# Kernel optimization log

Measured on AMD Instinct MI355X. Metric: run time of the kernel, lower is better.

## Reference

```python
import jax, jax.numpy as jnp
import numpy as np

B, S, D, H = 2, 2048, 2048, 16
HD = D // H  # 128


def setup_inputs() -> dict:
    key = jax.random.key(0)
    ks = jax.random.split(key, 6)
    sc = 0.02
    return {
        "x": jax.random.normal(ks[0], (B, S, D), jnp.float32),
        "attention_mask": jnp.ones((B, S), jnp.int32),
        "w_qkv": jax.random.normal(ks[1], (D, 3 * D), jnp.float32) * sc,
        "b_qkv": jnp.zeros((3 * D,), jnp.float32),
        "w_o": jax.random.normal(ks[2], (D, D), jnp.float32) * sc,
        "b_o": jnp.zeros((D,), jnp.float32),
        "ln1_w": jnp.ones((D,), jnp.float32),
        "w1": jax.random.normal(ks[3], (D, 8 * D), jnp.float32) * sc,
        "b1": jnp.zeros((8 * D,), jnp.float32),
        "w2": jax.random.normal(ks[4], (4 * D, D), jnp.float32) * sc,
        "b2": jnp.zeros((D,), jnp.float32),
        "ln2_w": jnp.ones((D,), jnp.float32),
    }


def rmsnorm(x, w, eps=1e-6):
    rms = jnp.sqrt(jnp.mean(x * x, axis=-1, keepdims=True) + eps)
    return w * (x / rms)


def rope_tables(seq_len, dim, base=10000.0):
    inv_freq = 1.0 / (base ** (jnp.arange(0, dim, 2, dtype=jnp.float32) / dim))
    t = jnp.arange(seq_len, dtype=jnp.float32)
    freqs = t[:, None] * inv_freq[None, :]          # [S, dim/2]
    emb = jnp.concatenate([freqs, freqs], axis=-1)  # [S, dim]
    return jnp.cos(emb), jnp.sin(emb)


def apply_rope(x, cos, sin):
    # Faithful to source: rotate pairs, then out = rot*cos + roll(rot,1)*sin
    xr = x.reshape(*x.shape[:-1], -1, 2)
    x1, x2 = xr[..., 0], xr[..., 1]
    rot = jnp.stack([-x2, x1], axis=-1).reshape(x.shape)
    return rot * cos + jnp.roll(rot, shift=1, axis=-1) * sin


def transformer_layer(x, attention_mask, w_qkv, b_qkv, w_o, b_o, ln1_w, w1, b1, w2, b2, ln2_w):
    residual = x
    qkv = x @ w_qkv + b_qkv                         # [B,S,3D]
    q, k, v = jnp.split(qkv, 3, axis=-1)
    split = lambda t: t.reshape(B, S, H, HD).transpose(0, 2, 1, 3)  # [B,H,S,HD]
    q, k, v = split(q), split(k), split(v)

    cos, sin = rope_tables(S, HD)                   # [S,HD], broadcasts over B,H
    q = apply_rope(q, cos, sin)
    k = apply_rope(k, cos, sin)

    scores = jnp.einsum("bhqd,bhkd->bhqk", q, k) / jnp.sqrt(jnp.float32(HD))
    mask = (attention_mask == 1)[:, None, None, :]  # [B,1,1,S]
    scores = jnp.where(mask, scores, -jnp.inf)
    attn = jax.nn.softmax(scores, axis=-1)
    out = jnp.einsum("bhqk,bhkd->bhqd", attn, v)
    out = out.transpose(0, 2, 1, 3).reshape(B, S, D)
    out = out @ w_o + b_o

    x = rmsnorm(out + residual, ln1_w)
    residual = x
    h = x @ w1 + b1                                 # [B,S,8D]
    h, gate = jnp.split(h, 2, axis=-1)
    h = h * jax.nn.gelu(gate, approximate=False)
    h = h @ w2 + b2
    return rmsnorm(h + residual, ln2_w)


def reference(x, attention_mask, w_qkv, b_qkv, w_o, b_o, ln1_w, w1, b1, w2, b2, ln2_w):
    return transformer_layer(x, attention_mask, w_qkv, b_qkv, w_o, b_o, ln1_w, w1, b1, w2, b2, ln2_w)
```

## Files before the change

### kernel.cpp

```cpp
#include <hip/hip_runtime.h>
#include <cstdint>

typedef unsigned short u16;
typedef __attribute__((ext_vector_type(8))) short short8;
typedef __attribute__((ext_vector_type(8))) unsigned short ushortx8;
typedef __attribute__((ext_vector_type(4))) float floatx4;

#define DEV __device__ __forceinline__

DEV u16 f2bf(float f) {
  union { float f; uint32_t u; } x; x.f = f;
  uint32_t r = x.u + 0x7fffu + ((x.u >> 16) & 1u);
  return (u16)(r >> 16);
}
DEV float bf2f(u16 h) {
  union { float f; uint32_t u; } x; x.u = ((uint32_t)h) << 16;
  return x.f;
}
DEV float fast_gelu(float g) {
  float u = 0.7978845608f * (g + 0.044715f * g * g * g);
  float e = __expf(-2.0f * fabsf(u));
  float th = (1.0f - e) / (1.0f + e);
  th = (u < 0.0f) ? -th : th;
  return 0.5f * g * (1.0f + th);
}
DEV void gload_lds16(const void* g, void* lds) {
  __builtin_amdgcn_global_load_lds(
      (const __attribute__((address_space(1))) char*)(uintptr_t)g,
      (__attribute__((address_space(3))) char*)(uintptr_t)lds, 16, 0, 0);
}


__global__ __launch_bounds__(256) void k_cvt_bf16(const float* __restrict__ in,
                                                  u16* __restrict__ out, int n) {
  int i = (blockIdx.x * 256 + threadIdx.x) * 4;
  if (i + 3 < n) {
    float4 v = *(const float4*)(in + i);
    ushort4 o;
    o.x = f2bf(v.x); o.y = f2bf(v.y); o.z = f2bf(v.z); o.w = f2bf(v.w);
    *(ushort4*)(out + i) = o;
  }
}

__global__ __launch_bounds__(256) void k_transpose_all(const float* __restrict__ Wq,
                                                       u16* __restrict__ WqT,
                                                       const float* __restrict__ Wo,
                                                       u16* __restrict__ WoT,
                                                       const float* __restrict__ W2,
                                                       u16* __restrict__ W2T) {
  __shared__ u16 t[32][33];
  int id = blockIdx.x;
  const float* W; u16* Wt; int R, C, tix;
  if (id < 12288)      { W = Wq; Wt = WqT; R = 2048; C = 6144; tix = id; }
  else if (id < 16384) { W = Wo; Wt = WoT; R = 2048; C = 2048; tix = id - 12288; }
  else                 { W = W2; Wt = W2T; R = 8192; C = 2048; tix = id - 16384; }
  int ntc = C >> 5;
  int c0 = (tix % ntc) * 32, r0 = (tix / ntc) * 32;
  int tx = threadIdx.x & 31, ty = threadIdx.x >> 5;
#pragma unroll
  for (int i = ty; i < 32; i += 8)
    t[i][tx] = f2bf(W[(size_t)(r0 + i) * C + c0 + tx]);
  __syncthreads();
#pragma unroll
  for (int i = ty; i < 32; i += 8)
    Wt[(size_t)(c0 + i) * R + r0 + tx] = t[tx][i];
}

__global__ __launch_bounds__(256) void k_transpose_w1p(const float* __restrict__ W,
                                                       u16* __restrict__ Wt) {
  __shared__ u16 t[32][33];
  int tx = threadIdx.x & 31, ty = threadIdx.x >> 5;
  int r0 = blockIdx.y * 32;
  int c0 = blockIdx.x * 32;
  int eta = c0 + tx;
  int Bq = eta >> 8, i = eta & 255, wn = (i >> 6) & 3, r = i & 63, n = r >> 4, tt = r & 15;
  int src = Bq * 128 + wn * 32 + (n & 1) * 16 + tt + ((n >= 2) ? 8192 : 0);
#pragma unroll
  for (int k = ty; k < 32; k += 8)
    t[k][tx] = f2bf(W[(size_t)(r0 + k) * 16384 + src]);
  __syncthreads();
#pragma unroll
  for (int i2 = ty; i2 < 32; i2 += 8)
    Wt[(size_t)(c0 + i2) * 2048 + r0 + tx] = t[tx][i2];
}

__global__ __launch_bounds__(256) void k_rope_tab(float* __restrict__ ct, float* __restrict__ st) {
  int i = blockIdx.x * 256 + threadIdx.x;
  int s = i >> 6, j = i & 63;
  float invf = 1.0f / powf(10000.0f, (float)j * (1.0f / 64.0f));
  float ang = (float)s * invf;
  ct[i] = cosf(ang);
  st[i] = sinf(ang);
}

__global__ __launch_bounds__(256) void k_rope_split(const u16* __restrict__ qkv,
                                                    const float* __restrict__ ct,
                                                    const float* __restrict__ st,
                                                    u16* __restrict__ qr, u16* __restrict__ kr) {
  int bs = blockIdx.x;
  int b = bs >> 11, s = bs & 2047;
  __shared__ float q[2048], k[2048];
  const u16* row = qkv + (size_t)bs * 6144;
  for (int i = threadIdx.x * 4; i < 2048; i += 1024) {
    ushort4 qa = *(const ushort4*)(row + i);
    ushort4 ka = *(const ushort4*)(row + 2048 + i);
    q[i] = bf2f(qa.x); q[i + 1] = bf2f(qa.y); q[i + 2] = bf2f(qa.z); q[i + 3] = bf2f(qa.w);
    k[i] = bf2f(ka.x); k[i + 1] = bf2f(ka.y); k[i + 2] = bf2f(ka.z); k[i + 3] = bf2f(ka.w);
  }
  __syncthreads();
  int i0 = threadIdx.x * 8;
  int h = i0 >> 7, d0 = i0 & 127;
  const float* qh = q + (h << 7);
  const float* kh = k + (h << 7);
  ushortx8 qo, ko;
#pragma unroll
  for (int e = 0; e < 8; ++e) {
    int d = d0 + e;
    int dm1 = (d + 127) & 127;
    float c = ct[(s << 6) + (d & 63)];
    float sn = st[(s << 6) + (d & 63)];
    float rq  = (d & 1)   ? qh[d - 1]   : -qh[d + 1];
    float rq1 = (dm1 & 1) ? qh[dm1 - 1] : -qh[dm1 + 1];
    float rk  = (d & 1)   ? kh[d - 1]   : -kh[d + 1];
    float rk1 = (dm1 & 1) ? kh[dm1 - 1] : -kh[dm1 + 1];
    qo[e] = f2bf(rq * c + rq1 * sn);
    ko[e] = f2bf(rk * c + rk1 * sn);
  }
  size_t obase = (((size_t)b * 16 + h) * 2048 + s) * 128 + d0;
  *(ushortx8*)(qr + obase) = qo;
  *(ushortx8*)(kr + obase) = ko;
}

__global__ __launch_bounds__(256) void k_v_transpose(const u16* __restrict__ qkv,
                                                     u16* __restrict__ vt) {
  __shared__ u16 t[32][33];
  int tx = threadIdx.x & 31, ty = threadIdx.x >> 5;
  int s0 = blockIdx.x * 32;
  int dm0 = (blockIdx.y & 63) * 32;
  int b = blockIdx.y >> 6;
#pragma unroll
  for (int i = ty; i < 32; i += 8)
    t[i][tx] = qkv[((size_t)(b * 2048) + s0 + i) * 6144 + 4096 + dm0 + tx];
  __syncthreads();
#pragma unroll
  for (int i = ty; i < 32; i += 8)
    vt[((size_t)b * 2048 + dm0 + i) * 2048 + s0 + tx] = t[tx][i];
}

template <int EPI>
__global__ __launch_bounds__(512, 2) void k_gemm256(const u16* __restrict__ A,
                                                    const u16* __restrict__ Bt,
                                                    void* __restrict__ C,
                                                    const float* __restrict__ bias,
                                                    int M, int N, int K, int nsplit) {
  __shared__ __align__(16) u16 lds[4][2][8192];
  const int tid = threadIdx.x;
  const int w = tid >> 6, lane = tid & 63;
  const int l15 = lane & 15, l4 = lane >> 4;
  const int wm = w >> 2, wn = w & 3;
  const int nbn = N >> 8;
  const int nbm = M >> 8;

  int bm, bn, split = 0;
  if (nsplit == 1 && nbm == 16 && (nbn & 7) == 0) {
    const int xcd = blockIdx.x & 7, l = blockIdx.x >> 3;
    const int xr = xcd >> 1, xc = xcd & 1;
    const int stn = l >> 4, lbm = (l >> 2) & 3, lbn = l & 3;
    bm = xr * 4 + lbm;
    bn = xc * (nbn >> 1) + stn * 4 + lbn;
  } else {
    const int nwg = gridDim.x;
    const int q = nwg >> 3, r8 = nwg & 7;
    const int xcd = blockIdx.x & 7, loc = blockIdx.x >> 3;
    const int swz = (xcd < r8 ? xcd * (q + 1) : r8 * (q + 1) + (xcd - r8) * q) + loc;
    const int ntiles = nwg / nsplit;
    split = swz / ntiles;
    const int tix = swz % ntiles;
    bm = tix / nbn; bn = tix % nbn;
  }
  const int klen = K / nsplit;
  const int kofs = split * klen;

  const size_t abase = (size_t)bm * 256 * K + kofs;
  const size_t bbase = (size_t)bn * 256 * K + kofs;
  const int nt = klen >> 5;

  const int sr = tid >> 2;
  const int sc = (tid & 3) ^ ((sr >> 1) & 3);
  auto stage = [&](int kt, int li, int op) {
    const u16* src = op ? (Bt + bbase) : (A + abase);
    gload_lds16(src + (size_t)(li * 128 + sr) * K + kt * 32 + sc * 8,
                (void*)&lds[kt & 3][op][(li * 512 + w * 64) * 8]);
  };

  const int fro = l15 * 32 + (l4 ^ ((l15 >> 1) & 3)) * 8;

  floatx4 acc[8][4];
  floatx4 zero = {0.f, 0.f, 0.f, 0.f};
#pragma unroll
  for (int m = 0; m < 8; ++m)
#pragma unroll
    for (int n = 0; n < 4; ++n) acc[m][n] = zero;

  for (int kt = 0; kt < 3; ++kt)
    if (kt < nt) {
      stage(kt, 0, 0); stage(kt, 0, 1);
      stage(kt, 1, 0); stage(kt, 1, 1);
    }

  for (int t = 0; t < nt; ++t) {
    const int buf = t & 3;
    if (t < nt - 2)       asm volatile("s_waitcnt vmcnt(8)" ::: "memory");
    else if (t == nt - 2) asm volatile("s_waitcnt vmcnt(4)" ::: "memory");
    else                  asm volatile("s_waitcnt vmcnt(0)" ::: "memory");
    __builtin_amdgcn_sched_barrier(0);
    __builtin_amdgcn_s_barrier();
    const u16* Ab = &lds[buf][0][wm * 4096 + fro];
    const u16* Bb = &lds[buf][1][wn * 2048 + fro];
    short8 av[4], bv[4];
#pragma unroll
    for (int n = 0; n < 4; ++n) bv[n] = *(const short8*)(Bb + n * 512);
#pragma unroll
    for (int i = 0; i < 4; ++i) av[i] = *(const short8*)(Ab + i * 512);
    if (t + 3 < nt) { stage(t + 3, 0, 0); stage(t + 3, 0, 1); }
    asm volatile("s_waitcnt lgkmcnt(0)" ::: "memory");
    __builtin_amdgcn_sched_barrier(0);
    __builtin_amdgcn_s_setprio(1);
#pragma unroll
    for (int i = 0; i < 4; ++i)
#pragma unroll
      for (int n = 0; n < 4; ++n)
        acc[i][n] = __builtin_amdgcn_mfma_f32_16x16x32_bf16(av[i], bv[n], acc[i][n], 0, 0, 0);
    __builtin_amdgcn_s_setprio(0);
    __builtin_amdgcn_s_barrier();
#pragma unroll
    for (int i = 0; i < 4; ++i) av[i] = *(const short8*)(Ab + (4 + i) * 512);
    if (t + 3 < nt) { stage(t + 3, 1, 0); stage(t + 3, 1, 1); }
    asm volatile("s_waitcnt lgkmcnt(0)" ::: "memory");
    __builtin_amdgcn_sched_barrier(0);
    __builtin_amdgcn_s_setprio(1);
#pragma unroll
    for (int i = 0; i < 4; ++i)
#pragma unroll
      for (int n = 0; n < 4; ++n)
        acc[4 + i][n] = __builtin_amdgcn_mfma_f32_16x16x32_bf16(av[i], bv[n], acc[4 + i][n], 0, 0, 0);
    __builtin_amdgcn_s_setprio(0);
  }

  const int row0 = bm * 256 + wm * 128, col0 = bn * 256 + wn * 64;
  if (EPI == 2) {
    float* P = (float*)C + (size_t)split * M * N;
#pragma unroll
    for (int n = 0; n < 4; ++n) {
      int col = col0 + n * 16 + l15;
#pragma unroll
      for (int m = 0; m < 8; ++m)
#pragma unroll
        for (int j = 0; j < 4; ++j) {
          int row = row0 + m * 16 + l4 * 4 + j;
          P[(size_t)row * N + col] = acc[m][n][j];
        }
    }
  } else if (EPI == 3) {
    __syncthreads();
    u16* ep = ((u16*)lds) + w * 4096;
    const int colA = bn * 128 + wn * 32;
#pragma unroll
    for (int n = 0; n < 2; ++n) {
      float ba = bias[colA + n * 16 + l15];
      float bg = bias[8192 + colA + n * 16 + l15];
#pragma unroll
      for (int m = 0; m < 8; ++m)
#pragma unroll
        for (int j = 0; j < 4; ++j) {
          float a = acc[m][n][j] + ba;
          float g = acc[m][n + 2][j] + bg;
          ep[(m * 16 + l4 * 4 + j) * 32 + n * 16 + l15] = f2bf(a * fast_gelu(g));
        }
    }
    const int rr = lane >> 2, cg = lane & 3;
    u16* Cg = (u16*)C;
    const int Nact = N >> 1;
#pragma unroll
    for (int pass = 0; pass < 8; ++pass) {
      short8 v = *(const short8*)&ep[(pass * 16 + rr) * 32 + cg * 8];
      size_t grow = row0 + pass * 16 + rr;
      *(short8*)&Cg[grow * Nact + colA + cg * 8] = v;
    }
  } else {
    __syncthreads();
    u16* ep = ((u16*)lds) + w * 8192;
#pragma unroll
    for (int n = 0; n < 4; ++n) {
      float bb = bias[col0 + n * 16 + l15];
#pragma unroll
      for (int m = 0; m < 8; ++m)
#pragma unroll
        for (int j = 0; j < 4; ++j)
          ep[(m * 16 + l4 * 4 + j) * 64 + n * 16 + l15] = f2bf(acc[m][n][j] + bb);
    }
    const int rr = lane >> 3, cg = lane & 7;
    u16* Cg = (u16*)C;
#pragma unroll
    for (int pass = 0; pass < 16; ++pass) {
      short8 v = *(const short8*)&ep[(pass * 8 + rr) * 64 + cg * 8];
      size_t grow = row0 + pass * 8 + rr;
      *(short8*)&Cg[grow * N + col0 + cg * 8] = v;
    }
  }
}

__global__ __launch_bounds__(512, 4) void k_attn(const u16* __restrict__ Qr,
                                                 const u16* __restrict__ Kr,
                                                 const u16* __restrict__ Vt,
                                                 const int* __restrict__ mask,
                                                 u16* __restrict__ O) {
  constexpr int S = 2048, HD = 128, H = 16;
  __shared__ __align__(16) u16 Ksh[64 * 128];
  __shared__ __align__(16) u16 Vsh[128 * 64];
  __shared__ __align__(16) u16 Psh[8][16 * 72];
  __shared__ float Msh[2048];

  const int bid = blockIdx.x;
  const int xcd = bid & 7, local = bid >> 3;
  const int bh = xcd * 4 + (local >> 4);
  const int qt = local & 15;
  const int b = bh >> 4, h = bh & 15;
  const int tid = threadIdx.x, wave = tid >> 6, lane = tid & 63;
  const int l15 = lane & 15, l4 = lane >> 4;
  const size_t bhs = (size_t)(b * H + h);
  const u16* Qb = Qr + bhs * S * HD;
  const u16* Kb = Kr + bhs * S * HD;
  const u16* Vb = Vt + bhs * HD * S;

  for (int i = tid; i < 2048; i += 512)
    Msh[i] = (mask[b * S + i] == 1) ? 0.0f : -1e30f;

  const int qrow = qt * 128 + wave * 16 + l15;
  short8 qf[4];
#pragma unroll
  for (int kk = 0; kk < 4; ++kk)
    qf[kk] = *(const short8*)&Qb[(size_t)qrow * HD + kk * 32 + l4 * 8];

  float m_run[4], l_run[4];
  floatx4 o_acc[8];
  floatx4 zero = {0.f, 0.f, 0.f, 0.f};
#pragma unroll
  for (int j = 0; j < 4; ++j) { m_run[j] = -1e30f; l_run[j] = 0.f; }
#pragma unroll
  for (int n = 0; n < 8; ++n) o_acc[n] = zero;

  for (int ktile = 0; ktile < S / 64; ++ktile) {
    __syncthreads();
#pragma unroll
    for (int it = 0; it < 2; ++it) {
      int gi = it * 512 + tid;
      {
        int row = gi >> 4, g = gi & 15;
        int gs = (g & 8) | ((g ^ row) & 7);
        gload_lds16(Kb + (size_t)(ktile * 64 + row) * HD + gs * 8,
                    (char*)&Ksh[it * 4096 + wave * 512]);
      }
      {
        int row = gi >> 3, g = gi & 7;
        int gs = (g ^ row) & 7;
        gload_lds16(Vb + (size_t)row * S + ktile * 64 + gs * 8,
                    (char*)&Vsh[it * 4096 + wave * 512]);
      }
    }
    __syncthreads();

    floatx4 s_acc[4];
#pragma unroll
    for (int nf = 0; nf < 4; ++nf) s_acc[nf] = zero;
    __builtin_amdgcn_s_setprio(1);
#pragma unroll
    for (int kk = 0; kk < 4; ++kk) {
#pragma unroll
      for (int nf = 0; nf < 4; ++nf) {
        int key = nf * 16 + l15;
        int G = kk * 4 + l4;
        int lg = (G & 8) | ((G ^ key) & 7);
        short8 kv = *(const short8*)&Ksh[key * 128 + lg * 8];
        s_acc[nf] = __builtin_amdgcn_mfma_f32_16x16x32_bf16(qf[kk], kv, s_acc[nf], 0, 0, 0);
      }
    }
    __builtin_amdgcn_s_setprio(0);

    const float scale = 0.08838834764831845f;
    float p[4][4];
#pragma unroll
    for (int nf = 0; nf < 4; ++nf) {
      float ma = Msh[ktile * 64 + nf * 16 + l15];
#pragma unroll
      for (int j = 0; j < 4; ++j) p[nf][j] = s_acc[nf][j] * scale + ma;
    }
#pragma unroll
    for (int j = 0; j < 4; ++j) {
      float mx = fmaxf(fmaxf(p[0][j], p[1][j]), fmaxf(p[2][j], p[3][j]));
      mx = fmaxf(mx, __shfl_xor(mx, 1));
      mx = fmaxf(mx, __shfl_xor(mx, 2));
      mx = fmaxf(mx, __shfl_xor(mx, 4));
      mx = fmaxf(mx, __shfl_xor(mx, 8));
      float mnew = fmaxf(m_run[j], mx);
      float corr = __expf(m_run[j] - mnew);
      float ps = 0.f;
#pragma unroll
      for (int nf = 0; nf < 4; ++nf) {
        p[nf][j] = __expf(p[nf][j] - mnew);
        ps += p[nf][j];
      }
      l_run[j] = l_run[j] * corr + ps;
      m_run[j] = mnew;
#pragma unroll
      for (int n = 0; n < 8; ++n) o_acc[n][j] *= corr;
    }

#pragma unroll
    for (int nf = 0; nf < 4; ++nf)
#pragma unroll
      for (int j = 0; j < 4; ++j)
        Psh[wave][(l4 * 4 + j) * 72 + nf * 16 + l15] = f2bf(p[nf][j]);

    __builtin_amdgcn_s_setprio(1);
#pragma unroll
    for (int ks = 0; ks < 2; ++ks) {
      short8 pa = *(const short8*)&Psh[wave][l15 * 72 + ks * 32 + l4 * 8];
#pragma unroll
      for (int nf2 = 0; nf2 < 8; ++nf2) {
        int hd = nf2 * 16 + l15;
        int G = ks * 4 + l4;
        short8 vv = *(const short8*)&Vsh[hd * 64 + ((G ^ hd) & 7) * 8];
        o_acc[nf2] = __builtin_amdgcn_mfma_f32_16x16x32_bf16(pa, vv, o_acc[nf2], 0, 0, 0);
      }
    }
    __builtin_amdgcn_s_setprio(0);
  }

#pragma unroll
  for (int j = 0; j < 4; ++j) {
    float ls = l_run[j];
    ls += __shfl_xor(ls, 1); ls += __shfl_xor(ls, 2);
    ls += __shfl_xor(ls, 4); ls += __shfl_xor(ls, 8);
    l_run[j] = ls;
  }

#pragma unroll
  for (int j = 0; j < 4; ++j) {
    float inv = 1.0f / l_run[j];
    int srow = qt * 128 + wave * 16 + l4 * 4 + j;
    size_t orow = ((size_t)b * S + srow) * 2048 + h * 128;
#pragma unroll
    for (int nf2 = 0; nf2 < 8; ++nf2)
      O[orow + nf2 * 16 + l15] = f2bf(o_acc[nf2][j] * inv);
  }
}

template <int OUTMODE>
__global__ __launch_bounds__(256) void k_rms_fuse(const float* __restrict__ p0,
                                                  const float* __restrict__ p1,
                                                  const float* __restrict__ bias,
                                                  const float* __restrict__ resid,
                                                  const float* __restrict__ w,
                                                  u16* __restrict__ ob,
                                                  float* __restrict__ of) {
  int row = blockIdx.x;
  int t = threadIdx.x;
  size_t base = (size_t)row * 2048 + t * 8;
  float4 a0 = *(const float4*)(p0 + base);
  float4 a1 = *(const float4*)(p0 + base + 4);
  float4 b0 = *(const float4*)(p1 + base);
  float4 b1 = *(const float4*)(p1 + base + 4);
  float4 r0 = *(const float4*)(resid + base);
  float4 r1 = *(const float4*)(resid + base + 4);
  float4 c0 = *(const float4*)(bias + t * 8);
  float4 c1 = *(const float4*)(bias + t * 8 + 4);
  float v[8];
  v[0] = a0.x + b0.x + r0.x + c0.x; v[1] = a0.y + b0.y + r0.y + c0.y;
  v[2] = a0.z + b0.z + r0.z + c0.z; v[3] = a0.w + b0.w + r0.w + c0.w;
  v[4] = a1.x + b1.x + r1.x + c1.x; v[5] = a1.y + b1.y + r1.y + c1.y;
  v[6] = a1.z + b1.z + r1.z + c1.z; v[7] = a1.w + b1.w + r1.w + c1.w;
  float ss = 0.f;
#pragma unroll
  for (int e = 0; e < 8; ++e) ss += v[e] * v[e];
#pragma unroll
  for (int d = 1; d < 64; d <<= 1) ss += __shfl_xor(ss, d);
  __shared__ float sred[4];
  if ((t & 63) == 0) sred[t >> 6] = ss;
  __syncthreads();
  float tot = sred[0] + sred[1] + sred[2] + sred[3];
  float scale = rsqrtf(tot * (1.0f / 2048.0f) + 1e-6f);
  const float* wp = w + t * 8;
  float o[8];
#pragma unroll
  for (int e = 0; e < 8; ++e) o[e] = v[e] * wp[e] * scale;
  if (OUTMODE == 1) {
    ushort4 q0, q1;
    q0.x = f2bf(o[0]); q0.y = f2bf(o[1]); q0.z = f2bf(o[2]); q0.w = f2bf(o[3]);
    q1.x = f2bf(o[4]); q1.y = f2bf(o[5]); q1.z = f2bf(o[6]); q1.w = f2bf(o[7]);
    *(ushort4*)(ob + base) = q0;
    *(ushort4*)(ob + base + 4) = q1;
  }
  {
    float4 f0, f1;
    f0.x = o[0]; f0.y = o[1]; f0.z = o[2]; f0.w = o[3];
    f1.x = o[4]; f1.y = o[5]; f1.z = o[6]; f1.w = o[7];
    *(float4*)(of + base) = f0;
    *(float4*)(of + base + 4) = f1;
  }
}

extern "C" void kernel_launch(void* const* d_in, const int* in_sizes, int n_in,
                              void* d_out, int out_size, void* d_ws, size_t ws_size,
                              hipStream_t stream) {
  const float* x     = (const float*)d_in[0];
  const int*   amask = (const int*)d_in[1];
  const float* w_qkv = (const float*)d_in[2];
  const float* b_qkv = (const float*)d_in[3];
  const float* w_o   = (const float*)d_in[4];
  const float* b_o   = (const float*)d_in[5];
  const float* ln1_w = (const float*)d_in[6];
  const float* w1    = (const float*)d_in[7];
  const float* b1    = (const float*)d_in[8];
  const float* w2    = (const float*)d_in[9];
  const float* b2    = (const float*)d_in[10];
  const float* ln2_w = (const float*)d_in[11];
  float* out = (float*)d_out;

  char* ws = (char*)d_ws;
  u16*   xb    = (u16*)(ws + 0);
  u16*   wqkvT = (u16*)(ws + 16777216);
  u16*   woT   = (u16*)(ws + 41943040);
  u16*   w1Tp  = (u16*)(ws + 50331648);
  u16*   w2T   = (u16*)(ws + 117440512);
  float* ctab  = (float*)(ws + 150994944);
  float* stab  = (float*)(ws + 151519232);
  u16*   qkv   = (u16*)(ws + 152043520);
  u16*   qr    = (u16*)(ws + 202375168);
  u16*   kr    = (u16*)(ws + 219152384);
  u16*   vt    = (u16*)(ws + 235929600);
  u16*   aout  = (u16*)(ws + 252706816);
  u16*   x1b   = (u16*)(ws + 303038464);
  float* x1f   = (float*)(ws + 319815680);
  float* p01a  = (float*)(ws + 152043520);
  u16*   act   = (u16*)(ws + 152043520);
  float* p01b  = (float*)(ws + 219152384);

  k_cvt_bf16<<<8192, 256, 0, stream>>>(x, xb, 4096 * 2048);
  k_transpose_all<<<32768, 256, 0, stream>>>(w_qkv, wqkvT, w_o, woT, w2, w2T);
  k_transpose_w1p<<<dim3(512, 64), 256, 0, stream>>>(w1, w1Tp);
  k_rope_tab<<<512, 256, 0, stream>>>(ctab, stab);

  k_gemm256<0><<<16 * 24, 512, 0, stream>>>(xb, wqkvT, qkv, b_qkv, 4096, 6144, 2048, 1);
  k_rope_split<<<4096, 256, 0, stream>>>(qkv, ctab, stab, qr, kr);
  k_v_transpose<<<dim3(64, 128), 256, 0, stream>>>(qkv, vt);
  k_attn<<<512, 512, 0, stream>>>(qr, kr, vt, amask, aout);

  k_gemm256<2><<<16 * 8 * 2, 512, 0, stream>>>(aout, woT, p01a, nullptr, 4096, 2048, 2048, 2);
  k_rms_fuse<1><<<4096, 256, 0, stream>>>(p01a, p01a + (size_t)4096 * 2048, b_o, x, ln1_w, x1b, x1f);

  k_gemm256<3><<<16 * 64, 512, 0, stream>>>(x1b, w1Tp, act, b1, 4096, 16384, 2048, 1);

  k_gemm256<2><<<16 * 8 * 2, 512, 0, stream>>>(act, w2T, p01b, nullptr, 4096, 2048, 8192, 2);
  k_rms_fuse<2><<<4096, 256, 0, stream>>>(p01b, p01b + (size_t)4096 * 2048, b2, x1f, ln2_w, nullptr, out);
}
```

Measured before the change: 897.2 us.

## Fuse RoPE and V transpose into QKV GEMM epilogue; drop fp32 residual copy

Adds a new GEMM epilogue that stages each 256x256 QKV tile in LDS, then either applies RoPE and writes Q/K in head-major layout or transposes V directly into the vt buffer. This removes the separate rope_split and v_transpose kernels and the write and reread of the bf16 qkv intermediate. The RMS-norm kernel is also split into two variants: the second reads the bf16 residual x1b instead of an fp32 copy, which saves a 32MB write and read. The cost is a slightly lower-precision residual in the second norm and a longer, two-phase epilogue with extra synchronisation inside the GEMM.

Result: faster. 870.9 us (-2.9%).

```diff
diff --git a/kernel.cpp b/kernel.cpp
--- a/kernel.cpp
+++ b/kernel.cpp
@@ -93,66 +93,17 @@
   st[i] = sinf(ang);
 }
 
-__global__ __launch_bounds__(256) void k_rope_split(const u16* __restrict__ qkv,
-                                                    const float* __restrict__ ct,
-                                                    const float* __restrict__ st,
-                                                    u16* __restrict__ qr, u16* __restrict__ kr) {
-  int bs = blockIdx.x;
-  int b = bs >> 11, s = bs & 2047;
-  __shared__ float q[2048], k[2048];
-  const u16* row = qkv + (size_t)bs * 6144;
-  for (int i = threadIdx.x * 4; i < 2048; i += 1024) {
-    ushort4 qa = *(const ushort4*)(row + i);
-    ushort4 ka = *(const ushort4*)(row + 2048 + i);
-    q[i] = bf2f(qa.x); q[i + 1] = bf2f(qa.y); q[i + 2] = bf2f(qa.z); q[i + 3] = bf2f(qa.w);
-    k[i] = bf2f(ka.x); k[i + 1] = bf2f(ka.y); k[i + 2] = bf2f(ka.z); k[i + 3] = bf2f(ka.w);
-  }
-  __syncthreads();
-  int i0 = threadIdx.x * 8;
-  int h = i0 >> 7, d0 = i0 & 127;
-  const float* qh = q + (h << 7);
-  const float* kh = k + (h << 7);
-  ushortx8 qo, ko;
-#pragma unroll
-  for (int e = 0; e < 8; ++e) {
-    int d = d0 + e;
-    int dm1 = (d + 127) & 127;
-    float c = ct[(s << 6) + (d & 63)];
-    float sn = st[(s << 6) + (d & 63)];
-    float rq  = (d & 1)   ? qh[d - 1]   : -qh[d + 1];
-    float rq1 = (dm1 & 1) ? qh[dm1 - 1] : -qh[dm1 + 1];
-    float rk  = (d & 1)   ? kh[d - 1]   : -kh[d + 1];
-    float rk1 = (dm1 & 1) ? kh[dm1 - 1] : -kh[dm1 + 1];
-    qo[e] = f2bf(rq * c + rq1 * sn);
-    ko[e] = f2bf(rk * c + rk1 * sn);
-  }
-  size_t obase = (((size_t)b * 16 + h) * 2048 + s) * 128 + d0;
-  *(ushortx8*)(qr + obase) = qo;
-  *(ushortx8*)(kr + obase) = ko;
-}
-
-__global__ __launch_bounds__(256) void k_v_transpose(const u16* __restrict__ qkv,
-                                                     u16* __restrict__ vt) {
-  __shared__ u16 t[32][33];
-  int tx = threadIdx.x & 31, ty = threadIdx.x >> 5;
-  int s0 = blockIdx.x * 32;
-  int dm0 = (blockIdx.y & 63) * 32;
-  int b = blockIdx.y >> 6;
-#pragma unroll
-  for (int i = ty; i < 32; i += 8)
-    t[i][tx] = qkv[((size_t)(b * 2048) + s0 + i) * 6144 + 4096 + dm0 + tx];
-  __syncthreads();
-#pragma unroll
-  for (int i = ty; i < 32; i += 8)
-    vt[((size_t)b * 2048 + dm0 + i) * 2048 + s0 + tx] = t[tx][i];
-}
-
 template <int EPI>
 __global__ __launch_bounds__(512, 2) void k_gemm256(const u16* __restrict__ A,
                                                     const u16* __restrict__ Bt,
                                                     void* __restrict__ C,
                                                     const float* __restrict__ bias,
-                                                    int M, int N, int K, int nsplit) {
+                                                    int M, int N, int K, int nsplit,
+                                                    u16* __restrict__ qrO,
+                                                    u16* __restrict__ krO,
+                                                    u16* __restrict__ vtO,
+                                                    const float* __restrict__ ctabO,
+                                                    const float* __restrict__ stabO) {
   __shared__ __align__(16) u16 lds[4][2][8192];
   const int tid = threadIdx.x;
   const int w = tid >> 6, lane = tid & 63;
@@ -287,6 +238,76 @@
       size_t grow = row0 + pass * 16 + rr;
       *(short8*)&Cg[grow * Nact + colA + cg * 8] = v;
     }
+  } else if (EPI == 4) {
+    constexpr int PAD = 264;
+    u16* T = (u16*)lds;
+    const int bq = bm >> 3;
+    const int srow0 = (bm & 7) * 256;
+#pragma unroll 1
+    for (int hf = 0; hf < 2; ++hf) {
+      __syncthreads();
+      if (wm == hf) {
+#pragma unroll
+        for (int n = 0; n < 4; ++n) {
+          float bb = bias[bn * 256 + wn * 64 + n * 16 + l15];
+#pragma unroll
+          for (int m = 0; m < 8; ++m)
+#pragma unroll
+            for (int j = 0; j < 4; ++j)
+              T[(m * 16 + l4 * 4 + j) * PAD + wn * 64 + n * 16 + l15] =
+                  f2bf(acc[m][n][j] + bb);
+        }
+      }
+      __syncthreads();
+      if (bn < 16) {
+        int sl = tid >> 2, hh = (tid >> 1) & 1, t2 = tid & 1;
+        const u16* row = T + sl * PAD + hh * 128;
+        int s = srow0 + hf * 128 + sl;
+        int head = 2 * (bn & 7) + hh;
+        u16* dst = (bn < 8 ? qrO : krO) +
+                   (((size_t)bq * 16 + head) * 2048 + s) * 128 + t2 * 64;
+        const float* ctr = ctabO + (s << 6);
+        const float* str2 = stabO + (s << 6);
+#pragma unroll
+        for (int ch = 0; ch < 8; ++ch) {
+          int d0 = t2 * 64 + ch * 8;
+          ushortx8 xv = *(const ushortx8*)(row + d0);
+          float xp = bf2f(row[(d0 + 126) & 127]);
+          int f0 = d0 & 63;
+          float4 c0v = *(const float4*)(ctr + f0);
+          float4 c1v = *(const float4*)(ctr + f0 + 4);
+          float4 s0v = *(const float4*)(str2 + f0);
+          float4 s1v = *(const float4*)(str2 + f0 + 4);
+          float cc[8] = {c0v.x, c0v.y, c0v.z, c0v.w, c1v.x, c1v.y, c1v.z, c1v.w};
+          float sn[8] = {s0v.x, s0v.y, s0v.z, s0v.w, s1v.x, s1v.y, s1v.z, s1v.w};
+          ushortx8 o;
+#pragma unroll
+          for (int pr = 0; pr < 4; ++pr) {
+            float xe = bf2f((u16)xv[2 * pr]), xo = bf2f((u16)xv[2 * pr + 1]);
+            o[2 * pr]     = f2bf(-xo * cc[2 * pr] + xp * sn[2 * pr]);
+            o[2 * pr + 1] = f2bf( xe * cc[2 * pr + 1] - xo * sn[2 * pr + 1]);
+            xp = xe;
+          }
+          *(ushortx8*)(dst + ch * 8) = o;
+        }
+      } else {
+        int hh = tid >> 8, dg = (tid >> 4) & 15, sc2 = tid & 15;
+        int head = 2 * (bn - 16) + hh;
+        int s0 = srow0 + hf * 128 + sc2 * 8;
+        ushortx8 r[8];
+#pragma unroll
+        for (int i = 0; i < 8; ++i)
+          r[i] = *(const ushortx8*)(T + (sc2 * 8 + i) * PAD + hh * 128 + dg * 8);
+        u16* vbase = vtO + ((size_t)bq * 2048 + head * 128 + dg * 8) * 2048 + s0;
+#pragma unroll
+        for (int j2 = 0; j2 < 8; ++j2) {
+          ushortx8 o;
+#pragma unroll
+          for (int i = 0; i < 8; ++i) o[i] = r[i][j2];
+          *(ushortx8*)(vbase + (size_t)j2 * 2048) = o;
+        }
+      }
+    }
   } else {
     __syncthreads();
     u16* ep = ((u16*)lds) + w * 8192;
@@ -456,14 +477,12 @@
   }
 }
 
-template <int OUTMODE>
-__global__ __launch_bounds__(256) void k_rms_fuse(const float* __restrict__ p0,
-                                                  const float* __restrict__ p1,
-                                                  const float* __restrict__ bias,
-                                                  const float* __restrict__ resid,
-                                                  const float* __restrict__ w,
-                                                  u16* __restrict__ ob,
-                                                  float* __restrict__ of) {
+__global__ __launch_bounds__(256) void k_rms_fuse1(const float* __restrict__ p0,
+                                                   const float* __restrict__ p1,
+                                                   const float* __restrict__ bias,
+                                                   const float* __restrict__ resid,
+                                                   const float* __restrict__ w,
+                                                   u16* __restrict__ ob) {
   int row = blockIdx.x;
   int t = threadIdx.x;
   size_t base = (size_t)row * 2048 + t * 8;
@@ -491,23 +510,56 @@
   float tot = sred[0] + sred[1] + sred[2] + sred[3];
   float scale = rsqrtf(tot * (1.0f / 2048.0f) + 1e-6f);
   const float* wp = w + t * 8;
-  float o[8];
-#pragma unroll
-  for (int e = 0; e < 8; ++e) o[e] = v[e] * wp[e] * scale;
-  if (OUTMODE == 1) {
-    ushort4 q0, q1;
-    q0.x = f2bf(o[0]); q0.y = f2bf(o[1]); q0.z = f2bf(o[2]); q0.w = f2bf(o[3]);
-    q1.x = f2bf(o[4]); q1.y = f2bf(o[5]); q1.z = f2bf(o[6]); q1.w = f2bf(o[7]);
-    *(ushort4*)(ob + base) = q0;
-    *(ushort4*)(ob + base + 4) = q1;
-  }
-  {
-    float4 f0, f1;
-    f0.x = o[0]; f0.y = o[1]; f0.z = o[2]; f0.w = o[3];
-    f1.x = o[4]; f1.y = o[5]; f1.z = o[6]; f1.w = o[7];
-    *(float4*)(of + base) = f0;
-    *(float4*)(of + base + 4) = f1;
-  }
+  ushort4 q0, q1;
+  q0.x = f2bf(v[0] * wp[0] * scale); q0.y = f2bf(v[1] * wp[1] * scale);
+  q0.z = f2bf(v[2] * wp[2] * scale); q0.w = f2bf(v[3] * wp[3] * scale);
+  q1.x = f2bf(v[4] * wp[4] * scale); q1.y = f2bf(v[5] * wp[5] * scale);
+  q1.z = f2bf(v[6] * wp[6] * scale); q1.w = f2bf(v[7] * wp[7] * scale);
+  *(ushort4*)(ob + base) = q0;
+  *(ushort4*)(ob + base + 4) = q1;
+}
+
+__global__ __launch_bounds__(256) void k_rms_fuse2(const float* __restrict__ p0,
+                                                   const float* __restrict__ p1,
+                                                   const float* __restrict__ bias,
+                                                   const u16* __restrict__ residb,
+                                                   const float* __restrict__ w,
+                                                   float* __restrict__ of) {
+  int row = blockIdx.x;
+  int t = threadIdx.x;
+  size_t base = (size_t)row * 2048 + t * 8;
+  float4 a0 = *(const float4*)(p0 + base);
+  float4 a1 = *(const float4*)(p0 + base + 4);
+  float4 b0 = *(const float4*)(p1 + base);
+  float4 b1 = *(const float4*)(p1 + base + 4);
+  ushortx8 rb = *(const ushortx8*)(residb + base);
+  float4 c0 = *(const float4*)(bias + t * 8);
+  float4 c1 = *(const float4*)(bias + t * 8 + 4);
+  float v[8];
+  v[0] = a0.x + b0.x + c0.x; v[1] = a0.y + b0.y + c0.y;
+  v[2] = a0.z + b0.z + c0.z; v[3] = a0.w + b0.w + c0.w;
+  v[4] = a1.x + b1.x + c1.x; v[5] = a1.y + b1.y + c1.y;
+  v[6] = a1.z + b1.z + c1.z; v[7] = a1.w + b1.w + c1.w;
+#pragma unroll
+  for (int e = 0; e < 8; ++e) v[e] += bf2f((u16)rb[e]);
+  float ss = 0.f;
+#pragma unroll
+  for (int e = 0; e < 8; ++e) ss += v[e] * v[e];
+#pragma unroll
+  for (int d = 1; d < 64; d <<= 1) ss += __shfl_xor(ss, d);
+  __shared__ float sred[4];
+  if ((t & 63) == 0) sred[t >> 6] = ss;
+  __syncthreads();
+  float tot = sred[0] + sred[1] + sred[2] + sred[3];
+  float scale = rsqrtf(tot * (1.0f / 2048.0f) + 1e-6f);
+  const float* wp = w + t * 8;
+  float4 f0, f1;
+  f0.x = v[0] * wp[0] * scale; f0.y = v[1] * wp[1] * scale;
+  f0.z = v[2] * wp[2] * scale; f0.w = v[3] * wp[3] * scale;
+  f1.x = v[4] * wp[4] * scale; f1.y = v[5] * wp[5] * scale;
+  f1.z = v[6] * wp[6] * scale; f1.w = v[7] * wp[7] * scale;
+  *(float4*)(of + base) = f0;
+  *(float4*)(of + base + 4) = f1;
 }
 
 extern "C" void kernel_launch(void* const* d_in, const int* in_sizes, int n_in,
@@ -535,13 +587,11 @@
   u16*   w2T   = (u16*)(ws + 117440512);
   float* ctab  = (float*)(ws + 150994944);
   float* stab  = (float*)(ws + 151519232);
-  u16*   qkv   = (u16*)(ws + 152043520);
   u16*   qr    = (u16*)(ws + 202375168);
   u16*   kr    = (u16*)(ws + 219152384);
   u16*   vt    = (u16*)(ws + 235929600);
   u16*   aout  = (u16*)(ws + 252706816);
   u16*   x1b   = (u16*)(ws + 303038464);
-  float* x1f   = (float*)(ws + 319815680);
   float* p01a  = (float*)(ws + 152043520);
   u16*   act   = (u16*)(ws + 152043520);
   float* p01b  = (float*)(ws + 219152384);
@@ -551,16 +601,22 @@
   k_transpose_w1p<<<dim3(512, 64), 256, 0, stream>>>(w1, w1Tp);
   k_rope_tab<<<512, 256, 0, stream>>>(ctab, stab);
 
-  k_gemm256<0><<<16 * 24, 512, 0, stream>>>(xb, wqkvT, qkv, b_qkv, 4096, 6144, 2048, 1);
-  k_rope_split<<<4096, 256, 0, stream>>>(qkv, ctab, stab, qr, kr);
-  k_v_transpose<<<dim3(64, 128), 256, 0, stream>>>(qkv, vt);
+  k_gemm256<4><<<16 * 24, 512, 0, stream>>>(xb, wqkvT, nullptr, b_qkv,
+                                            4096, 6144, 2048, 1,
+                                            qr, kr, vt, ctab, stab);
   k_attn<<<512, 512, 0, stream>>>(qr, kr, vt, amask, aout);
 
-  k_gemm256<2><<<16 * 8 * 2, 512, 0, stream>>>(aout, woT, p01a, nullptr, 4096, 2048, 2048, 2);
-  k_rms_fuse<1><<<4096, 256, 0, stream>>>(p01a, p01a + (size_t)4096 * 2048, b_o, x, ln1_w, x1b, x1f);
-
-  k_gemm256<3><<<16 * 64, 512, 0, stream>>>(x1b, w1Tp, act, b1, 4096, 16384, 2048, 1);
-
-  k_gemm256<2><<<16 * 8 * 2, 512, 0, stream>>>(act, w2T, p01b, nullptr, 4096, 2048, 8192, 2);
-  k_rms_fuse<2><<<4096, 256, 0, stream>>>(p01b, p01b + (size_t)4096 * 2048, b2, x1f, ln2_w, nullptr, out);
-}
+  k_gemm256<2><<<16 * 8 * 2, 512, 0, stream>>>(aout, woT, p01a, nullptr,
+                                               4096, 2048, 2048, 2,
+                                               nullptr, nullptr, nullptr, nullptr, nullptr);
+  k_rms_fuse1<<<4096, 256, 0, stream>>>(p01a, p01a + (size_t)4096 * 2048, b_o, x, ln1_w, x1b);
+
+  k_gemm256<3><<<16 * 64, 512, 0, stream>>>(x1b, w1Tp, act, b1,
+                                            4096, 16384, 2048, 1,
+                                            nullptr, nullptr, nullptr, nullptr, nullptr);
+
+  k_gemm256<2><<<16 * 8 * 2, 512, 0, stream>>>(act, w2T, p01b, nullptr,
+                                               4096, 2048, 8192, 2,
+                                               nullptr, nullptr, nullptr, nullptr, nullptr);
+  k_rms_fuse2<<<4096, 256, 0, stream>>>(p01b, p01b + (size_t)4096 * 2048, b2, x1b, ln2_w, out);
+}
```
